# Kernel optimization log

Hardware: AMD Instinct MI355X
Metric: run time of the kernel (lower is better)

The kernel has to match this reference:

```python
import jax, jax.numpy as jnp
import numpy as np

C_S = 384; C_Z = 256; HD = 16; NH = 12; NQ = 4; NV = 8; L = 512
WC = float(np.sqrt(2.0 / (9.0 * NQ)))
WL = float(np.sqrt(1.0 / 3.0))


def quat2rot(q):
    # q: [L,4] -> R: [L,3,3] (normalized quaternion to rotation matrix)
    q = q / jnp.linalg.norm(q, axis=-1, keepdims=True)
    w, x, y, z = q[..., 0], q[..., 1], q[..., 2], q[..., 3]
    R = jnp.stack([
        1 - 2 * (y * y + z * z), 2 * (x * y - w * z), 2 * (x * z + w * y),
        2 * (x * y + w * z), 1 - 2 * (x * x + z * z), 2 * (y * z - w * x),
        2 * (x * z - w * y), 2 * (y * z + w * x), 1 - 2 * (x * x + y * y)
    ], axis=-1)
    return R.reshape(q.shape[:-1] + (3, 3))


def _layer_norm(x, g, b, eps=1e-5):
    m = x.mean(-1, keepdims=True)
    v = x.var(-1, keepdims=True)
    return (x - m) / jnp.sqrt(v + eps) * g + b


def setup_inputs() -> dict:
    key = jax.random.key(0)
    ks = jax.random.split(key, 20)
    f32 = jnp.float32
    def w(k, shape, fan_in):
        return (jax.random.normal(k, shape) / np.sqrt(fan_in)).astype(f32)
    shid = NH * (C_Z + HD + NV * 3 + NV)  # 3648
    return {
        "s": jax.random.normal(ks[0], (1, L, C_S), f32),
        "z": jax.random.normal(ks[1], (1, L, L, C_Z), f32),
        "quat_tns": jax.random.normal(ks[2], (1, L, 4), f32),
        "trsl_tns": jax.random.normal(ks[3], (1, L, 3), f32),
        "Wq": w(ks[4], (C_S, NH * HD), C_S),
        "Wk": w(ks[5], (C_S, NH * HD), C_S),
        "Wv": w(ks[6], (C_S, NH * HD), C_S),
        "Wqp": w(ks[7], (C_S, NH * NQ * 3), C_S),
        "Wkp": w(ks[8], (C_S, NH * NQ * 3), C_S),
        "Wvp": w(ks[9], (C_S, NH * NV * 3), C_S),
        "Wb": w(ks[10], (C_Z, NH), C_Z),
        "Ws": w(ks[11], (shid, C_S), shid),
        "bs": jnp.zeros((C_S,), f32),
        "scale": jnp.full((NH,), np.log(np.e - 1.0), f32),
        "g1": jnp.ones((C_S,), f32), "b1": jnp.zeros((C_S,), f32),
        "Wm1": w(ks[12], (C_S, C_S), C_S), "bm1": jnp.zeros((C_S,), f32),
        "Wm2": w(ks[13], (C_S, C_S), C_S), "bm2": jnp.zeros((C_S,), f32),
        "Wm3": w(ks[14], (C_S, C_S), C_S), "bm3": jnp.zeros((C_S,), f32),
        "g2": jnp.ones((C_S,), f32), "b2": jnp.zeros((C_S,), f32),
    }


def reference(s, z, quat_tns, trsl_tns, Wq, Wk, Wv, Wqp, Wkp, Wvp, Wb, Ws, bs,
              scale, g1, b1, Wm1, bm1, Wm2, bm2, Wm3, bm3, g2, b2):
    N, Lr, _ = s.shape
    q = (s @ Wq).reshape(N, Lr, NH, HD)
    k = (s @ Wk).reshape(N, Lr, NH, HD)
    v = (s @ Wv).reshape(N, Lr, NH, HD)
    qp = (s @ Wqp).reshape(N, Lr, NH, NQ, 3)
    kp = (s @ Wkp).reshape(N, Lr, NH, NQ, 3)
    vp = (s @ Wvp).reshape(N, Lr, NH, NV, 3)
    b = z @ Wb                                   # [N,L,L,H]
    R = quat2rot(quat_tns[0])[None]              # [1,L,3,3]
    t = trsl_tns[:, :, None, None, :]            # [1,L,1,1,3]

    def fwd_trans(x):                            # global frame: R x + t
        return jnp.einsum('nlij,nlhpj->nlhpi', R, x) + t

    qpp = fwd_trans(qp)                          # [N,L,H,Q,3]
    kpp = fwd_trans(kp)
    vpp = fwd_trans(vp)                          # [N,L,H,V,3]

    # sum over points and coords of squared distances -> [N,L,L,H]
    d2 = jnp.sum((qpp[:, :, None] - kpp[:, None, :]) ** 2, axis=(-1, -2))
    qk = jnp.einsum('nihd,njhd->nijh', q, k) / np.sqrt(HD)
    qkp = 0.5 * WC * jax.nn.softplus(scale)[None, None, None, :] * d2
    a = jax.nn.softmax(WL * (qk + b - qkp), axis=2)  # softmax over keys j

    op = jnp.einsum('nijh,nijc->nihc', a, z)         # [N,L,H,C_Z]
    ov = jnp.einsum('nijh,njhd->nihd', a, v)         # [N,L,H,HD]
    ovp_g = jnp.einsum('nijh,njhp->nihp', a, vpp.reshape(N, Lr, NH, NV * 3))
    ovp_g = ovp_g.reshape(N, Lr, NH, NV, 3)
    # inverse transform: R^T (y - t)
    ovp = jnp.einsum('nlji,nlhvj->nlhvi', R, ovp_g - t)
    ovp_norm = jnp.linalg.norm(ovp, axis=-1)         # [N,L,H,V]

    shid = jnp.concatenate(
        [op, ov, ovp.reshape(N, Lr, NH, NV * 3), ovp_norm], axis=3
    ).reshape(N, Lr, -1)
    s1 = _layer_norm(s + shid @ Ws + bs, g1, b1)
    h = jax.nn.relu(s1 @ Wm1 + bm1)
    h = jax.nn.relu(h @ Wm2 + bm2)
    h = h @ Wm3 + bm3
    return _layer_norm(s1 + h, g2, b2)
```

## Files before the change

kernel.cpp:

```cpp
#include <hip/hip_runtime.h>
#include <math.h>

#define LSEQ 512
#define CS 384
#define CZ 256
#define HD 16
#define NH 12
#define NQ 4
#define NV 8
#define NALL 1152
#define SHID 3648
#define OFF_Q 0
#define OFF_K 192
#define OFF_V 384
#define OFF_QP 576
#define OFF_KP 720
#define OFF_VP 864

#define WC_CONST 0.2357022603955158f
#define WL_CONST 0.5773502691896258f

typedef __attribute__((ext_vector_type(8))) short bf16x8;
typedef __attribute__((ext_vector_type(4))) float f32x4;

__device__ __forceinline__ short f2bf(float f) {
  unsigned u = __builtin_bit_cast(unsigned, f);
  unsigned r = (u + 0x7FFF + ((u >> 16) & 1)) >> 16;
  return (short)r;
}

__global__ void k_prep(const float* quat, const float* trsl, const float* scale,
                       const float* Wb, float* R, float* T, float* CH,
                       unsigned short* WBP) {
  int t = threadIdx.x;
  if (t < LSEQ) {
    float w = quat[t*4+0], x = quat[t*4+1], y = quat[t*4+2], z = quat[t*4+3];
    float inv = 1.0f / sqrtf(w*w + x*x + y*y + z*z);
    w *= inv; x *= inv; y *= inv; z *= inv;
    float* r = R + t*9;
    r[0] = 1.f - 2.f*(y*y + z*z); r[1] = 2.f*(x*y - w*z);       r[2] = 2.f*(x*z + w*y);
    r[3] = 2.f*(x*y + w*z);       r[4] = 1.f - 2.f*(x*x + z*z); r[5] = 2.f*(y*z - w*x);
    r[6] = 2.f*(x*z - w*y);       r[7] = 2.f*(y*z + w*x);       r[8] = 1.f - 2.f*(x*x + y*y);
    T[t*3+0] = trsl[t*3+0]; T[t*3+1] = trsl[t*3+1]; T[t*3+2] = trsl[t*3+2];
  }
  if (t < NH) {
    float sc = scale[t];
    float sp = (sc > 20.f) ? sc : logf(1.f + expf(sc));
    CH[t] = 0.5f * WC_CONST * sp;
  }
  if (t < CZ) {
    #pragma unroll
    for (int h = 0; h < 16; h++)
      WBP[t*16 + h] = (h < NH) ? (unsigned short)f2bf(Wb[t*NH + h]) : (unsigned short)0;
  }
}

__global__ void k_concat(const float* Wq, const float* Wk, const float* Wv,
                         const float* Wqp, const float* Wkp, const float* Wvp,
                         float* Wcat) {
  int idx = blockIdx.x * 256 + threadIdx.x;
  if (idx >= CS * NALL) return;
  int r = idx / NALL, c = idx % NALL;
  float v;
  if (c < 192)       v = Wq [r*192 + c];
  else if (c < 384)  v = Wk [r*192 + (c-192)];
  else if (c < 576)  v = Wv [r*192 + (c-384)];
  else if (c < 720)  v = Wqp[r*144 + (c-576)];
  else if (c < 864)  v = Wkp[r*144 + (c-720)];
  else               v = Wvp[r*288 + (c-864)];
  Wcat[idx] = v;
}

__global__ __launch_bounds__(256) void k_gemm(
    const float* A, const float* B, float* C, const float* bias,
    int K, int lda, int ldb, int ldc, int splitk, int relu, int reluA) {
  int ks = blockIdx.z;
  int Ksub = K / splitk;
  int kbeg = ks * Ksub, kend = kbeg + Ksub;

  __shared__ __align__(16) float As[16][68];
  __shared__ __align__(16) float Bs[16][68];
  int t = threadIdx.x;
  int m0 = blockIdx.y * 64, n0 = blockIdx.x * 64;
  int arow = t >> 2,  akq = (t & 3) * 4;
  int bkk  = t >> 4,  bnq = (t & 15) * 4;
  int ty = (t >> 4) * 4, tx = (t & 15) * 4;
  float acc[4][4];
  #pragma unroll
  for (int r = 0; r < 4; r++)
    #pragma unroll
    for (int c = 0; c < 4; c++) acc[r][c] = 0.f;

  const float* aptr  = A + (long)(m0 + arow) * lda + akq;
  const float* bbase = B + n0 + bnq;
  float4 av = *(const float4*)&aptr[kbeg];
  float4 bv = *(const float4*)&bbase[(long)(kbeg + bkk) * ldb];

  for (int kb = kbeg; kb < kend; kb += 16) {
    float4 a_cur = av, b_cur = bv;
    if (reluA) {
      a_cur.x = fmaxf(a_cur.x, 0.f); a_cur.y = fmaxf(a_cur.y, 0.f);
      a_cur.z = fmaxf(a_cur.z, 0.f); a_cur.w = fmaxf(a_cur.w, 0.f);
    }
    __syncthreads();
    As[akq+0][arow] = a_cur.x; As[akq+1][arow] = a_cur.y;
    As[akq+2][arow] = a_cur.z; As[akq+3][arow] = a_cur.w;
    *(float4*)&Bs[bkk][bnq] = b_cur;
    __syncthreads();
    if (kb + 16 < kend) {
      av = *(const float4*)&aptr[kb + 16];
      bv = *(const float4*)&bbase[(long)(kb + 16 + bkk) * ldb];
    }
    #pragma unroll
    for (int kk = 0; kk < 16; kk++) {
      float4 a4 = *(float4*)&As[kk][ty];
      float4 b4 = *(float4*)&Bs[kk][tx];
      acc[0][0] += a4.x*b4.x; acc[0][1] += a4.x*b4.y; acc[0][2] += a4.x*b4.z; acc[0][3] += a4.x*b4.w;
      acc[1][0] += a4.y*b4.x; acc[1][1] += a4.y*b4.y; acc[1][2] += a4.y*b4.z; acc[1][3] += a4.y*b4.w;
      acc[2][0] += a4.z*b4.x; acc[2][1] += a4.z*b4.y; acc[2][2] += a4.z*b4.z; acc[2][3] += a4.z*b4.w;
      acc[3][0] += a4.w*b4.x; acc[3][1] += a4.w*b4.y; acc[3][2] += a4.w*b4.z; acc[3][3] += a4.w*b4.w;
    }
  }

  if (splitk == 1) {
    #pragma unroll
    for (int r = 0; r < 4; r++) {
      int m = m0 + ty + r;
      #pragma unroll
      for (int c = 0; c < 4; c++) {
        int n = n0 + tx + c;
        float v = acc[r][c] + (bias ? bias[n] : 0.f);
        if (relu) v = fmaxf(v, 0.f);
        C[(long)m * ldc + n] = v;
      }
    }
  } else {
    #pragma unroll
    for (int r = 0; r < 4; r++) {
      int m = m0 + ty + r;
      #pragma unroll
      for (int c = 0; c < 4; c++) {
        int n = n0 + tx + c;
        float v = acc[r][c] + ((ks == 0 && bias) ? bias[n] : 0.f);
        atomicAdd(&C[(long)m * ldc + n], v);
      }
    }
  }
}

__global__ void k_trans(const float* P, const float* R, const float* T,
                        float* QPP, float* KT, float* KPT, float* VBT) {
  int task = blockIdx.y;
  int idx = blockIdx.x * 256 + threadIdx.x;
  if (idx >= LSEQ * NH) return;
  int h = idx / LSEQ, l = idx % LSEQ;
  const float* r = R + l*9;
  float t0 = T[l*3], t1 = T[l*3+1], t2 = T[l*3+2];
  const float* prow = P + (long)l * NALL;
  if (task == 0) {
    #pragma unroll
    for (int pq = 0; pq < NQ; pq++) {
      const float* x = prow + OFF_QP + h*12 + pq*3;
      float a = x[0], b = x[1], c = x[2];
      float* o = QPP + l*144 + h*12 + pq*3;
      o[0] = r[0]*a + r[1]*b + r[2]*c + t0;
      o[1] = r[3]*a + r[4]*b + r[5]*c + t1;
      o[2] = r[6]*a + r[7]*b + r[8]*c + t2;
    }
    #pragma unroll
    for (int d = 0; d < HD; d++)
      KT[(h*HD + d)*LSEQ + l] = prow[OFF_K + h*HD + d];
  } else if (task == 1) {
    #pragma unroll
    for (int pq = 0; pq < NQ; pq++) {
      const float* x = prow + OFF_KP + h*12 + pq*3;
      float a = x[0], b = x[1], c = x[2];
      KPT[(h*12 + pq*3 + 0)*LSEQ + l] = r[0]*a + r[1]*b + r[2]*c + t0;
      KPT[(h*12 + pq*3 + 1)*LSEQ + l] = r[3]*a + r[4]*b + r[5]*c + t1;
      KPT[(h*12 + pq*3 + 2)*LSEQ + l] = r[6]*a + r[7]*b + r[8]*c + t2;
    }
  } else {
    #pragma unroll
    for (int d = 0; d < 16; d++)
      VBT[((long)(h*40 + d))*LSEQ + l] = prow[OFF_V + h*16 + d];
    #pragma unroll
    for (int pv = 0; pv < NV; pv++) {
      const float* x = prow + OFF_VP + h*24 + pv*3;
      float a = x[0], b = x[1], c = x[2];
      VBT[((long)(h*40 + 16 + 3*pv + 0))*LSEQ + l] = r[0]*a + r[1]*b + r[2]*c + t0;
      VBT[((long)(h*40 + 16 + 3*pv + 1))*LSEQ + l] = r[3]*a + r[4]*b + r[5]*c + t1;
      VBT[((long)(h*40 + 16 + 3*pv + 2))*LSEQ + l] = r[6]*a + r[7]*b + r[8]*c + t2;
    }
  }
}

#define AI 2
__global__ __launch_bounds__(512) void k_logit(const float* P, const float* QPP,
    const float* KT, const float* KPT, const float* CH, float* LG) {
  int i0 = blockIdx.x * AI;
  int t = threadIdx.x, j = t;
  #pragma unroll
  for (int h = 0; h < NH; h++) {
    float kreg[16];
    #pragma unroll
    for (int d = 0; d < 16; d++) kreg[d] = KT[(h*16 + d)*LSEQ + j];
    float kp[12];
    #pragma unroll
    for (int p = 0; p < 12; p++) kp[p] = KPT[(h*12 + p)*LSEQ + j];
    float ch = CH[h];
    #pragma unroll
    for (int ii = 0; ii < AI; ii++) {
      const float* q  = P + (long)(i0+ii)*NALL + OFF_Q + h*HD;
      const float* qp = QPP + (i0+ii)*144 + h*12;
      float dot = 0.f;
      #pragma unroll
      for (int d = 0; d < 16; d++) dot += q[d] * kreg[d];
      float d2 = 0.f;
      #pragma unroll
      for (int p = 0; p < 12; p++) { float dd = qp[p] - kp[p]; d2 += dd*dd; }
      LG[((long)(i0+ii)*NH + h)*LSEQ + j] = WL_CONST * (0.25f*dot - ch*d2);
    }
  }
}

__global__ __launch_bounds__(256) void k_fused(const float* zin,
    const unsigned short* WBP, const float* LG, const float* VBT,
    float* SH, float* OVT) {
  __shared__ __align__(16) float lgs[NH][520];
  __shared__ __align__(16) float es[NH][68];
  __shared__ float sred[4][NH];
  __shared__ float ssum[NH];
  int i = blockIdx.x, t = threadIdx.x;
  int w = t >> 6, l = t & 63;
  int r = l & 15, kg = l >> 4;

  const float* lgsrc = LG + (long)i * NH * LSEQ;
  #pragma unroll
  for (int idx = t; idx < NH*LSEQ/4; idx += 256) {
    int h = idx >> 7, q4 = idx & 127;
    *(float4*)&lgs[h][q4*4] = *(const float4*)&lgsrc[h*LSEQ + q4*4];
  }

  bf16x8 bfrag[8];
  #pragma unroll
  for (int kt = 0; kt < 8; kt++)
    #pragma unroll
    for (int jj = 0; jj < 8; jj++)
      bfrag[kt][jj] = (short)WBP[(kt*32 + kg*8 + jj)*16 + r];

  float accop[NH];
  #pragma unroll
  for (int h = 0; h < NH; h++) accop[h] = 0.f;
  int pair0 = t, pair1 = t + 256;
  int h0 = pair0 / 40, p0 = pair0 % 40;
  int h1 = pair1 / 40, p1 = pair1 % 40;
  float accv0 = 0.f, accv1 = 0.f;
  float sparts = 0.f;
  int hh = (r < NH) ? r : 0;

  __syncthreads();

  for (int jt = 0; jt < LSEQ; jt += 64) {
    int j0 = jt + w*16;
    const float* zrow = zin + ((long)i*LSEQ + j0 + r)*CZ + kg*8;
    f32x4 acc = {0.f, 0.f, 0.f, 0.f};
    #pragma unroll
    for (int kt = 0; kt < 8; kt++) {
      float4 z0 = *(const float4*)(zrow + kt*32);
      float4 z1 = *(const float4*)(zrow + kt*32 + 4);
      bf16x8 af;
      af[0] = f2bf(z0.x); af[1] = f2bf(z0.y); af[2] = f2bf(z0.z); af[3] = f2bf(z0.w);
      af[4] = f2bf(z1.x); af[5] = f2bf(z1.y); af[6] = f2bf(z1.z); af[7] = f2bf(z1.w);
      acc = __builtin_amdgcn_mfma_f32_16x16x32_bf16(af, bfrag[kt], acc, 0, 0, 0);
    }
    float4 lgv = *(float4*)&lgs[hh][j0 + kg*4];
    float e0 = __expf(lgv.x + WL_CONST*acc[0]);
    float e1 = __expf(lgv.y + WL_CONST*acc[1]);
    float e2 = __expf(lgv.z + WL_CONST*acc[2]);
    float e3 = __expf(lgv.w + WL_CONST*acc[3]);
    if (r < NH) {
      sparts += e0 + e1 + e2 + e3;
      *(float4*)&es[r][w*16 + kg*4] = make_float4(e0, e1, e2, e3);
    }
    __syncthreads();
    const float* zc = zin + ((long)i*LSEQ + jt)*CZ + t;
    #pragma unroll 4
    for (int jj = 0; jj < 64; jj += 4) {
      float z0 = zc[(jj+0)*CZ], z1 = zc[(jj+1)*CZ];
      float z2 = zc[(jj+2)*CZ], z3 = zc[(jj+3)*CZ];
      #pragma unroll
      for (int h = 0; h < NH; h++) {
        float4 ev = *(float4*)&es[h][jj];
        accop[h] += ev.x*z0 + ev.y*z1 + ev.z*z2 + ev.w*z3;
      }
    }
    {
      const float* vb0 = VBT + ((long)pair0)*LSEQ + jt;
      #pragma unroll
      for (int jj = 0; jj < 64; jj += 4) {
        float4 vv = *(const float4*)&vb0[jj];
        float4 ev = *(float4*)&es[h0][jj];
        accv0 += vv.x*ev.x + vv.y*ev.y + vv.z*ev.z + vv.w*ev.w;
      }
      if (pair1 < 480) {
        const float* vb1 = VBT + ((long)pair1)*LSEQ + jt;
        #pragma unroll
        for (int jj = 0; jj < 64; jj += 4) {
          float4 vv = *(const float4*)&vb1[jj];
          float4 ev = *(float4*)&es[h1][jj];
          accv1 += vv.x*ev.x + vv.y*ev.y + vv.z*ev.z + vv.w*ev.w;
        }
      }
    }
    __syncthreads();
  }

  sparts += __shfl_xor(sparts, 16);
  sparts += __shfl_xor(sparts, 32);
  if (l < NH) sred[w][l] = sparts;
  __syncthreads();
  if (t < NH) {
    float sv = sred[0][t] + sred[1][t] + sred[2][t] + sred[3][t];
    ssum[t] = 1.0f / sv;
  }
  __syncthreads();

  float* sh = SH + (long)i * SHID + t;
  #pragma unroll
  for (int h = 0; h < NH; h++) sh[h * 304] = accop[h] * ssum[h];
  OVT[(long)i*480 + pair0] = accv0 * ssum[h0];
  if (pair1 < 480) OVT[(long)i*480 + pair1] = accv1 * ssum[h1];
}

__global__ void k_ovp(const float* OVT, const float* R, const float* T, float* SH) {
  int idx = blockIdx.x * 256 + threadIdx.x;
  if (idx >= LSEQ * NH) return;
  int l = idx / NH, h = idx % NH;
  const float* o = OVT + (long)l*480 + h*40;
  float* sh = SH + (long)l * SHID + h * 304;
  #pragma unroll
  for (int d = 0; d < 16; d++) sh[256 + d] = o[d];
  const float* r = R + l*9;
  float t0 = T[l*3], t1 = T[l*3+1], t2 = T[l*3+2];
  #pragma unroll
  for (int v = 0; v < NV; v++) {
    float a = o[16+3*v+0] - t0, b = o[16+3*v+1] - t1, c = o[16+3*v+2] - t2;
    float x = r[0]*a + r[3]*b + r[6]*c;
    float y = r[1]*a + r[4]*b + r[7]*c;
    float zz= r[2]*a + r[5]*b + r[8]*c;
    sh[272 + 3*v + 0] = x;
    sh[272 + 3*v + 1] = y;
    sh[272 + 3*v + 2] = zz;
    sh[296 + v] = sqrtf(x*x + y*y + zz*zz);
  }
}

__global__ __launch_bounds__(384) void k_ln(const float* res, const float* y,
                                            const float* g, const float* b, float* out) {
  int l = blockIdx.x, t = threadIdx.x;
  __shared__ float red1[6], red2[6];
  __shared__ float mv[2];
  float x = res[(long)l * CS + t] + y[(long)l * CS + t];
  float s = x, s2 = x * x;
  #pragma unroll
  for (int off = 32; off >= 1; off >>= 1) { s += __shfl_xor(s, off); s2 += __shfl_xor(s2, off); }
  if ((t & 63) == 0) { red1[t >> 6] = s; red2[t >> 6] = s2; }
  __syncthreads();
  if (t == 0) {
    float ss = 0.f, ss2 = 0.f;
    #pragma unroll
    for (int u = 0; u < 6; u++) { ss += red1[u]; ss2 += red2[u]; }
    float m = ss / CS;
    float var = ss2 / CS - m * m;
    mv[0] = m; mv[1] = 1.0f / sqrtf(var + 1e-5f);
  }
  __syncthreads();
  out[(long)l * CS + t] = (x - mv[0]) * mv[1] * g[t] + b[t];
}

extern "C" void kernel_launch(void* const* d_in, const int* in_sizes, int n_in,
                              void* d_out, int out_size, void* d_ws, size_t ws_size,
                              hipStream_t stream) {
  const float* s    = (const float*)d_in[0];
  const float* z    = (const float*)d_in[1];
  const float* quat = (const float*)d_in[2];
  const float* trsl = (const float*)d_in[3];
  const float* Wq   = (const float*)d_in[4];
  const float* Wk   = (const float*)d_in[5];
  const float* Wv   = (const float*)d_in[6];
  const float* Wqp  = (const float*)d_in[7];
  const float* Wkp  = (const float*)d_in[8];
  const float* Wvp  = (const float*)d_in[9];
  const float* Wb   = (const float*)d_in[10];
  const float* Ws   = (const float*)d_in[11];
  const float* bs   = (const float*)d_in[12];
  const float* scale= (const float*)d_in[13];
  const float* g1   = (const float*)d_in[14];
  const float* b1   = (const float*)d_in[15];
  const float* Wm1  = (const float*)d_in[16];
  const float* bm1  = (const float*)d_in[17];
  const float* Wm2  = (const float*)d_in[18];
  const float* bm2  = (const float*)d_in[19];
  const float* Wm3  = (const float*)d_in[20];
  const float* bm3  = (const float*)d_in[21];
  const float* g2   = (const float*)d_in[22];
  const float* b2   = (const float*)d_in[23];
  float* out = (float*)d_out;

  float* p = (float*)d_ws;
  float* R    = p; p += 512*9;
  float* T    = p; p += 512*3;
  float* CH   = p; p += 16;
  unsigned short* WBP = (unsigned short*)p; p += (CZ*16)/2;
  float* Wcat = p; p += (long)CS*NALL;
  float* QPP  = p; p += LSEQ*144;
  float* KT   = p; p += NH*HD*LSEQ;
  float* KPT  = p; p += NH*12*LSEQ;
  float* VBT  = p; p += (long)NH*40*LSEQ;
  float* LG   = p; p += (long)LSEQ*NH*LSEQ;
  float* OVT  = p; p += (long)LSEQ*480;
  float* SH   = p; p += (long)LSEQ*SHID;
  float* S1   = p; p += LSEQ*CS;
  float* ZB   = p;
  float* P    = p; p += (long)LSEQ*NALL;
  float* T1   = p; p += LSEQ*CS;
  float* H1   = p; p += LSEQ*CS;
  float* H2   = p; p += LSEQ*CS;
  float* H3   = p; p += LSEQ*CS;
  size_t zbytes = ((size_t)LSEQ*NALL + 4*LSEQ*CS) * sizeof(float);

  hipMemsetAsync(ZB, 0, zbytes, stream);
  k_prep<<<1, 512, 0, stream>>>(quat, trsl, scale, Wb, R, T, CH, WBP);
  k_concat<<<(CS*NALL + 255)/256, 256, 0, stream>>>(Wq, Wk, Wv, Wqp, Wkp, Wvp, Wcat);
  k_gemm<<<dim3(NALL/64, LSEQ/64, 2), 256, 0, stream>>>(
      s, Wcat, P, nullptr, CS, CS, NALL, NALL, 2, 0, 0);
  k_trans<<<dim3(24, 3), 256, 0, stream>>>(P, R, T, QPP, KT, KPT, VBT);
  k_logit<<<LSEQ/AI, 512, 0, stream>>>(P, QPP, KT, KPT, CH, LG);
  k_fused<<<LSEQ, 256, 0, stream>>>(z, WBP, LG, VBT, SH, OVT);
  k_ovp<<<(LSEQ*NH + 255)/256, 256, 0, stream>>>(OVT, R, T, SH);
  k_gemm<<<dim3(CS/64, LSEQ/64, 12), 256, 0, stream>>>(
      SH, Ws, T1, bs, SHID, SHID, CS, CS, 12, 0, 0);
  k_ln<<<LSEQ, CS, 0, stream>>>(s, T1, g1, b1, S1);
  k_gemm<<<dim3(CS/64, LSEQ/64, 8), 256, 0, stream>>>(
      S1, Wm1, H1, bm1, CS, CS, CS, CS, 8, 0, 0);
  k_gemm<<<dim3(CS/64, LSEQ/64, 8), 256, 0, stream>>>(
      H1, Wm2, H2, bm2, CS, CS, CS, CS, 8, 0, 1);
  k_gemm<<<dim3(CS/64, LSEQ/64, 8), 256, 0, stream>>>(
      H2, Wm3, H3, bm3, CS, CS, CS, CS, 8, 0, 1);
  k_ln<<<LSEQ, CS, 0, stream>>>(S1, H3, g2, b2, out);
}
```

Measured before the change: 690.6 us.

## Split attention key dimension across two blocks with atomic accumulation

The fused attention/z-aggregation kernel now launches a 512x2 grid, each block handling half of the keys, and accumulates unnormalized outputs and softmax denominators via atomicAdd into zeroed buffers. A new normalization kernel divides op by the summed denominators, and k_ovp applies the same division to the value outputs. The logit kernel is also changed to one query row per block. This aims to raise occupancy and parallelism for the z-bound kernel, at the cost of atomics, a larger memset and an extra launch. It relies on no per-row max subtraction, which the code before also skipped.

```diff
diff --git a/kernel.cpp b/kernel.cpp
--- a/kernel.cpp
+++ b/kernel.cpp
@@ -194,11 +194,10 @@
   }
 }
 
-#define AI 2
 __global__ __launch_bounds__(512) void k_logit(const float* P, const float* QPP,
     const float* KT, const float* KPT, const float* CH, float* LG) {
-  int i0 = blockIdx.x * AI;
-  int t = threadIdx.x, j = t;
+  int i = blockIdx.x;
+  int j = threadIdx.x;
   #pragma unroll
   for (int h = 0; h < NH; h++) {
     float kreg[16];
@@ -208,36 +207,33 @@
     #pragma unroll
     for (int p = 0; p < 12; p++) kp[p] = KPT[(h*12 + p)*LSEQ + j];
     float ch = CH[h];
-    #pragma unroll
-    for (int ii = 0; ii < AI; ii++) {
-      const float* q  = P + (long)(i0+ii)*NALL + OFF_Q + h*HD;
-      const float* qp = QPP + (i0+ii)*144 + h*12;
-      float dot = 0.f;
-      #pragma unroll
-      for (int d = 0; d < 16; d++) dot += q[d] * kreg[d];
-      float d2 = 0.f;
-      #pragma unroll
-      for (int p = 0; p < 12; p++) { float dd = qp[p] - kp[p]; d2 += dd*dd; }
-      LG[((long)(i0+ii)*NH + h)*LSEQ + j] = WL_CONST * (0.25f*dot - ch*d2);
-    }
+    const float* q  = P + (long)i*NALL + OFF_Q + h*HD;
+    const float* qp = QPP + i*144 + h*12;
+    float dot = 0.f;
+    #pragma unroll
+    for (int d = 0; d < 16; d++) dot += q[d] * kreg[d];
+    float d2 = 0.f;
+    #pragma unroll
+    for (int p = 0; p < 12; p++) { float dd = qp[p] - kp[p]; d2 += dd*dd; }
+    LG[((long)i*NH + h)*LSEQ + j] = WL_CONST * (0.25f*dot - ch*d2);
   }
 }
 
 __global__ __launch_bounds__(256) void k_fused(const float* zin,
     const unsigned short* WBP, const float* LG, const float* VBT,
-    float* SH, float* OVT) {
-  __shared__ __align__(16) float lgs[NH][520];
+    float* SH, float* OVT, float* SSUM) {
+  __shared__ __align__(16) float lgs[NH][264];
   __shared__ __align__(16) float es[NH][68];
   __shared__ float sred[4][NH];
-  __shared__ float ssum[NH];
-  int i = blockIdx.x, t = threadIdx.x;
+  int i = blockIdx.x, js = blockIdx.y, t = threadIdx.x;
+  int jbase = js * 256;
   int w = t >> 6, l = t & 63;
   int r = l & 15, kg = l >> 4;
 
-  const float* lgsrc = LG + (long)i * NH * LSEQ;
-  #pragma unroll
-  for (int idx = t; idx < NH*LSEQ/4; idx += 256) {
-    int h = idx >> 7, q4 = idx & 127;
+  const float* lgsrc = LG + (long)i * NH * LSEQ + jbase;
+  #pragma unroll
+  for (int idx = t; idx < NH*256/4; idx += 256) {
+    int h = idx >> 6, q4 = idx & 63;
     *(float4*)&lgs[h][q4*4] = *(const float4*)&lgsrc[h*LSEQ + q4*4];
   }
 
@@ -252,17 +248,18 @@
   #pragma unroll
   for (int h = 0; h < NH; h++) accop[h] = 0.f;
   int pair0 = t, pair1 = t + 256;
-  int h0 = pair0 / 40, p0 = pair0 % 40;
-  int h1 = pair1 / 40, p1 = pair1 % 40;
+  int h0 = pair0 / 40;
+  int h1 = pair1 / 40;
   float accv0 = 0.f, accv1 = 0.f;
   float sparts = 0.f;
   int hh = (r < NH) ? r : 0;
 
   __syncthreads();
 
-  for (int jt = 0; jt < LSEQ; jt += 64) {
+  for (int jt = 0; jt < 256; jt += 64) {
     int j0 = jt + w*16;
-    const float* zrow = zin + ((long)i*LSEQ + j0 + r)*CZ + kg*8;
+    int j0g = jbase + j0;
+    const float* zrow = zin + ((long)i*LSEQ + j0g + r)*CZ + kg*8;
     f32x4 acc = {0.f, 0.f, 0.f, 0.f};
     #pragma unroll
     for (int kt = 0; kt < 8; kt++) {
@@ -283,7 +280,7 @@
       *(float4*)&es[r][w*16 + kg*4] = make_float4(e0, e1, e2, e3);
     }
     __syncthreads();
-    const float* zc = zin + ((long)i*LSEQ + jt)*CZ + t;
+    const float* zc = zin + ((long)i*LSEQ + jbase + jt)*CZ + t;
     #pragma unroll 4
     for (int jj = 0; jj < 64; jj += 4) {
       float z0 = zc[(jj+0)*CZ], z1 = zc[(jj+1)*CZ];
@@ -295,7 +292,7 @@
       }
     }
     {
-      const float* vb0 = VBT + ((long)pair0)*LSEQ + jt;
+      const float* vb0 = VBT + ((long)pair0)*LSEQ + jbase + jt;
       #pragma unroll
       for (int jj = 0; jj < 64; jj += 4) {
         float4 vv = *(const float4*)&vb0[jj];
@@ -303,7 +300,7 @@
         accv0 += vv.x*ev.x + vv.y*ev.y + vv.z*ev.z + vv.w*ev.w;
       }
       if (pair1 < 480) {
-        const float* vb1 = VBT + ((long)pair1)*LSEQ + jt;
+        const float* vb1 = VBT + ((long)pair1)*LSEQ + jbase + jt;
         #pragma unroll
         for (int jj = 0; jj < 64; jj += 4) {
           float4 vv = *(const float4*)&vb1[jj];
@@ -319,32 +316,41 @@
   sparts += __shfl_xor(sparts, 32);
   if (l < NH) sred[w][l] = sparts;
   __syncthreads();
-  if (t < NH) {
-    float sv = sred[0][t] + sred[1][t] + sred[2][t] + sred[3][t];
-    ssum[t] = 1.0f / sv;
-  }
-  __syncthreads();
+  if (t < NH)
+    atomicAdd(&SSUM[i*16 + t], sred[0][t] + sred[1][t] + sred[2][t] + sred[3][t]);
 
   float* sh = SH + (long)i * SHID + t;
   #pragma unroll
-  for (int h = 0; h < NH; h++) sh[h * 304] = accop[h] * ssum[h];
-  OVT[(long)i*480 + pair0] = accv0 * ssum[h0];
-  if (pair1 < 480) OVT[(long)i*480 + pair1] = accv1 * ssum[h1];
-}
-
-__global__ void k_ovp(const float* OVT, const float* R, const float* T, float* SH) {
+  for (int h = 0; h < NH; h++) atomicAdd(&sh[h * 304], accop[h]);
+  atomicAdd(&OVT[(long)i*480 + pair0], accv0);
+  if (pair1 < 480) atomicAdd(&OVT[(long)i*480 + pair1], accv1);
+}
+
+__global__ __launch_bounds__(256) void k_opnorm(const float* SSUM, float* SH) {
+  int i = blockIdx.x, t = threadIdx.x;
+  float* sh = SH + (long)i * SHID + t;
+  #pragma unroll
+  for (int h = 0; h < NH; h++) {
+    float inv = 1.0f / SSUM[i*16 + h];
+    sh[h * 304] *= inv;
+  }
+}
+
+__global__ void k_ovp(const float* OVT, const float* SSUM, const float* R,
+                      const float* T, float* SH) {
   int idx = blockIdx.x * 256 + threadIdx.x;
   if (idx >= LSEQ * NH) return;
   int l = idx / NH, h = idx % NH;
+  float inv = 1.0f / SSUM[l*16 + h];
   const float* o = OVT + (long)l*480 + h*40;
   float* sh = SH + (long)l * SHID + h * 304;
   #pragma unroll
-  for (int d = 0; d < 16; d++) sh[256 + d] = o[d];
+  for (int d = 0; d < 16; d++) sh[256 + d] = o[d] * inv;
   const float* r = R + l*9;
   float t0 = T[l*3], t1 = T[l*3+1], t2 = T[l*3+2];
   #pragma unroll
   for (int v = 0; v < NV; v++) {
-    float a = o[16+3*v+0] - t0, b = o[16+3*v+1] - t1, c = o[16+3*v+2] - t2;
+    float a = o[16+3*v+0]*inv - t0, b = o[16+3*v+1]*inv - t1, c = o[16+3*v+2]*inv - t2;
     float x = r[0]*a + r[3]*b + r[6]*c;
     float y = r[1]*a + r[4]*b + r[7]*c;
     float zz= r[2]*a + r[5]*b + r[8]*c;
@@ -418,8 +424,6 @@
   float* KPT  = p; p += NH*12*LSEQ;
   float* VBT  = p; p += (long)NH*40*LSEQ;
   float* LG   = p; p += (long)LSEQ*NH*LSEQ;
-  float* OVT  = p; p += (long)LSEQ*480;
-  float* SH   = p; p += (long)LSEQ*SHID;
   float* S1   = p; p += LSEQ*CS;
   float* ZB   = p;
   float* P    = p; p += (long)LSEQ*NALL;
@@ -427,7 +431,11 @@
   float* H1   = p; p += LSEQ*CS;
   float* H2   = p; p += LSEQ*CS;
   float* H3   = p; p += LSEQ*CS;
-  size_t zbytes = ((size_t)LSEQ*NALL + 4*LSEQ*CS) * sizeof(float);
+  float* SH   = p; p += (long)LSEQ*SHID;
+  float* OVT  = p; p += (long)LSEQ*480;
+  float* SSUM = p; p += LSEQ*16;
+  size_t zbytes = ((size_t)LSEQ*NALL + 4*LSEQ*CS + (size_t)LSEQ*SHID
+                   + (size_t)LSEQ*480 + LSEQ*16) * sizeof(float);
 
   hipMemsetAsync(ZB, 0, zbytes, stream);
   k_prep<<<1, 512, 0, stream>>>(quat, trsl, scale, Wb, R, T, CH, WBP);
@@ -435,9 +443,10 @@
   k_gemm<<<dim3(NALL/64, LSEQ/64, 2), 256, 0, stream>>>(
       s, Wcat, P, nullptr, CS, CS, NALL, NALL, 2, 0, 0);
   k_trans<<<dim3(24, 3), 256, 0, stream>>>(P, R, T, QPP, KT, KPT, VBT);
-  k_logit<<<LSEQ/AI, 512, 0, stream>>>(P, QPP, KT, KPT, CH, LG);
-  k_fused<<<LSEQ, 256, 0, stream>>>(z, WBP, LG, VBT, SH, OVT);
-  k_ovp<<<(LSEQ*NH + 255)/256, 256, 0, stream>>>(OVT, R, T, SH);
+  k_logit<<<LSEQ, 512, 0, stream>>>(P, QPP, KT, KPT, CH, LG);
+  k_fused<<<dim3(LSEQ, 2), 256, 0, stream>>>(z, WBP, LG, VBT, SH, OVT, SSUM);
+  k_opnorm<<<LSEQ, 256, 0, stream>>>(SSUM, SH);
+  k_ovp<<<(LSEQ*NH + 255)/256, 256, 0, stream>>>(OVT, SSUM, R, T, SH);
   k_gemm<<<dim3(CS/64, LSEQ/64, 12), 256, 0, stream>>>(
       SH, Ws, T1, bs, SHID, SHID, CS, CS, 12, 0, 0);
   k_ln<<<LSEQ, CS, 0, stream>>>(s, T1, g1, b1, S1);
```

Result: no change. 698.8 us (+1.2%).

## Fuse logit, attention and point-output kernels into one 512-thread kernel

Applied to the files above, without the earlier changes.

Folds the logit computation and the inverse-frame point transform into the main attention kernel, so the LG and OVT global intermediates and two launches are removed. Each block now has 512 threads split into two groups, each handling half of the key positions. The partial sums are combined through shared memory at the end. The per-step second barrier is replaced by double-buffered exp tiles. This removes the 12 MB logit round-trip, but each block now recomputes its own logits and needs more shared memory per block, which may lower occupancy.

```diff
diff --git a/kernel.cpp b/kernel.cpp
--- a/kernel.cpp
+++ b/kernel.cpp
@@ -194,51 +194,49 @@
   }
 }
 
-#define AI 2
-__global__ __launch_bounds__(512) void k_logit(const float* P, const float* QPP,
-    const float* KT, const float* KPT, const float* CH, float* LG) {
-  int i0 = blockIdx.x * AI;
-  int t = threadIdx.x, j = t;
-  #pragma unroll
-  for (int h = 0; h < NH; h++) {
-    float kreg[16];
-    #pragma unroll
-    for (int d = 0; d < 16; d++) kreg[d] = KT[(h*16 + d)*LSEQ + j];
-    float kp[12];
-    #pragma unroll
-    for (int p = 0; p < 12; p++) kp[p] = KPT[(h*12 + p)*LSEQ + j];
-    float ch = CH[h];
-    #pragma unroll
-    for (int ii = 0; ii < AI; ii++) {
-      const float* q  = P + (long)(i0+ii)*NALL + OFF_Q + h*HD;
-      const float* qp = QPP + (i0+ii)*144 + h*12;
+__global__ __launch_bounds__(512) void k_fused512(
+    const float* zin, const unsigned short* WBP, const float* P,
+    const float* QPP, const float* KT, const float* KPT, const float* CH,
+    const float* VBT, const float* R, const float* T, float* SH) {
+  __shared__ __align__(16) float smem[12864];
+  float (*lgs)[516] = (float (*)[516])smem;
+  float (*es)[2][NH][68] = (float (*)[2][NH][68])(smem + 6192);
+  float* sred   = smem + 6192 + 6528;
+  float* ssumv  = sred + 128;
+  float* red_op = smem + 6192;
+  float* red_v  = smem + 6192 + 3072;
+
+  int i = blockIdx.x, t = threadIdx.x;
+  int g = t >> 8;
+  int w8 = t >> 6;
+  int wg = w8 & 3;
+  int l = t & 63, r = l & 15, kg = l >> 4;
+  int cidx = t & 255;
+  int hh = (r < NH) ? r : 0;
+
+  {
+    int j = t;
+    const float* qb  = P + (long)i*NALL + OFF_Q;
+    const float* qpb = QPP + i*144;
+    #pragma unroll 2
+    for (int h = 0; h < NH; h++) {
+      float kreg[16];
+      #pragma unroll
+      for (int d = 0; d < 16; d++) kreg[d] = KT[(h*16 + d)*LSEQ + j];
+      float kp[12];
+      #pragma unroll
+      for (int p = 0; p < 12; p++) kp[p] = KPT[(h*12 + p)*LSEQ + j];
+      float ch = CH[h];
+      const float* q  = qb + h*HD;
+      const float* qp = qpb + h*12;
       float dot = 0.f;
       #pragma unroll
       for (int d = 0; d < 16; d++) dot += q[d] * kreg[d];
       float d2 = 0.f;
       #pragma unroll
       for (int p = 0; p < 12; p++) { float dd = qp[p] - kp[p]; d2 += dd*dd; }
-      LG[((long)(i0+ii)*NH + h)*LSEQ + j] = WL_CONST * (0.25f*dot - ch*d2);
-    }
-  }
-}
-
-__global__ __launch_bounds__(256) void k_fused(const float* zin,
-    const unsigned short* WBP, const float* LG, const float* VBT,
-    float* SH, float* OVT) {
-  __shared__ __align__(16) float lgs[NH][520];
-  __shared__ __align__(16) float es[NH][68];
-  __shared__ float sred[4][NH];
-  __shared__ float ssum[NH];
-  int i = blockIdx.x, t = threadIdx.x;
-  int w = t >> 6, l = t & 63;
-  int r = l & 15, kg = l >> 4;
-
-  const float* lgsrc = LG + (long)i * NH * LSEQ;
-  #pragma unroll
-  for (int idx = t; idx < NH*LSEQ/4; idx += 256) {
-    int h = idx >> 7, q4 = idx & 127;
-    *(float4*)&lgs[h][q4*4] = *(const float4*)&lgsrc[h*LSEQ + q4*4];
+      lgs[h][j] = WL_CONST * (0.25f*dot - ch*d2);
+    }
   }
 
   bf16x8 bfrag[8];
@@ -251,17 +249,17 @@
   float accop[NH];
   #pragma unroll
   for (int h = 0; h < NH; h++) accop[h] = 0.f;
-  int pair0 = t, pair1 = t + 256;
-  int h0 = pair0 / 40, p0 = pair0 % 40;
-  int h1 = pair1 / 40, p1 = pair1 % 40;
+  int pair0 = cidx, pair1 = cidx + 256;
+  int h0 = pair0 / 40, h1 = pair1 / 40;
   float accv0 = 0.f, accv1 = 0.f;
   float sparts = 0.f;
-  int hh = (r < NH) ? r : 0;
-
-  __syncthreads();
-
-  for (int jt = 0; jt < LSEQ; jt += 64) {
-    int j0 = jt + w*16;
+
+  __syncthreads();
+
+  int buf = 0;
+  for (int step = 0; step < 4; step++) {
+    int jt = step * 64;
+    int j0 = g*256 + jt + wg*16;
     const float* zrow = zin + ((long)i*LSEQ + j0 + r)*CZ + kg*8;
     f32x4 acc = {0.f, 0.f, 0.f, 0.f};
     #pragma unroll
@@ -280,78 +278,93 @@
     float e3 = __expf(lgv.w + WL_CONST*acc[3]);
     if (r < NH) {
       sparts += e0 + e1 + e2 + e3;
-      *(float4*)&es[r][w*16 + kg*4] = make_float4(e0, e1, e2, e3);
+      *(float4*)&es[g][buf][r][wg*16 + kg*4] = make_float4(e0, e1, e2, e3);
     }
     __syncthreads();
-    const float* zc = zin + ((long)i*LSEQ + jt)*CZ + t;
+    const float* zc = zin + ((long)i*LSEQ + g*256 + jt)*CZ + cidx;
     #pragma unroll 4
     for (int jj = 0; jj < 64; jj += 4) {
       float z0 = zc[(jj+0)*CZ], z1 = zc[(jj+1)*CZ];
       float z2 = zc[(jj+2)*CZ], z3 = zc[(jj+3)*CZ];
       #pragma unroll
       for (int h = 0; h < NH; h++) {
-        float4 ev = *(float4*)&es[h][jj];
+        float4 ev = *(float4*)&es[g][buf][h][jj];
         accop[h] += ev.x*z0 + ev.y*z1 + ev.z*z2 + ev.w*z3;
       }
     }
     {
-      const float* vb0 = VBT + ((long)pair0)*LSEQ + jt;
+      const float* vb0 = VBT + ((long)pair0)*LSEQ + g*256 + jt;
       #pragma unroll
       for (int jj = 0; jj < 64; jj += 4) {
         float4 vv = *(const float4*)&vb0[jj];
-        float4 ev = *(float4*)&es[h0][jj];
+        float4 ev = *(float4*)&es[g][buf][h0][jj];
         accv0 += vv.x*ev.x + vv.y*ev.y + vv.z*ev.z + vv.w*ev.w;
       }
       if (pair1 < 480) {
-        const float* vb1 = VBT + ((long)pair1)*LSEQ + jt;
+        const float* vb1 = VBT + ((long)pair1)*LSEQ + g*256 + jt;
         #pragma unroll
         for (int jj = 0; jj < 64; jj += 4) {
           float4 vv = *(const float4*)&vb1[jj];
-          float4 ev = *(float4*)&es[h1][jj];
+          float4 ev = *(float4*)&es[g][buf][h1][jj];
           accv1 += vv.x*ev.x + vv.y*ev.y + vv.z*ev.z + vv.w*ev.w;
         }
       }
     }
-    __syncthreads();
+    buf ^= 1;
   }
 
   sparts += __shfl_xor(sparts, 16);
   sparts += __shfl_xor(sparts, 32);
-  if (l < NH) sred[w][l] = sparts;
-  __syncthreads();
+  if (l < NH) sred[w8*16 + l] = sparts;
+  __syncthreads();
+
+  if (g == 1) {
+    #pragma unroll
+    for (int h = 0; h < NH; h++) red_op[h*256 + cidx] = accop[h];
+    red_v[pair0] = accv0;
+    if (pair1 < 480) red_v[pair1] = accv1;
+  }
   if (t < NH) {
-    float sv = sred[0][t] + sred[1][t] + sred[2][t] + sred[3][t];
-    ssum[t] = 1.0f / sv;
-  }
-  __syncthreads();
-
-  float* sh = SH + (long)i * SHID + t;
-  #pragma unroll
-  for (int h = 0; h < NH; h++) sh[h * 304] = accop[h] * ssum[h];
-  OVT[(long)i*480 + pair0] = accv0 * ssum[h0];
-  if (pair1 < 480) OVT[(long)i*480 + pair1] = accv1 * ssum[h1];
-}
-
-__global__ void k_ovp(const float* OVT, const float* R, const float* T, float* SH) {
-  int idx = blockIdx.x * 256 + threadIdx.x;
-  if (idx >= LSEQ * NH) return;
-  int l = idx / NH, h = idx % NH;
-  const float* o = OVT + (long)l*480 + h*40;
-  float* sh = SH + (long)l * SHID + h * 304;
-  #pragma unroll
-  for (int d = 0; d < 16; d++) sh[256 + d] = o[d];
-  const float* r = R + l*9;
-  float t0 = T[l*3], t1 = T[l*3+1], t2 = T[l*3+2];
-  #pragma unroll
-  for (int v = 0; v < NV; v++) {
-    float a = o[16+3*v+0] - t0, b = o[16+3*v+1] - t1, c = o[16+3*v+2] - t2;
-    float x = r[0]*a + r[3]*b + r[6]*c;
-    float y = r[1]*a + r[4]*b + r[7]*c;
-    float zz= r[2]*a + r[5]*b + r[8]*c;
-    sh[272 + 3*v + 0] = x;
-    sh[272 + 3*v + 1] = y;
-    sh[272 + 3*v + 2] = zz;
-    sh[296 + v] = sqrtf(x*x + y*y + zz*zz);
+    float sv = 0.f;
+    #pragma unroll
+    for (int u = 0; u < 8; u++) sv += sred[u*16 + t];
+    ssumv[t] = 1.0f / sv;
+  }
+  __syncthreads();
+
+  if (g == 0) {
+    float* sh = SH + (long)i * SHID + cidx;
+    #pragma unroll
+    for (int h = 0; h < NH; h++)
+      sh[h * 304] = (accop[h] + red_op[h*256 + cidx]) * ssumv[h];
+    float v0 = (accv0 + red_v[pair0]) * ssumv[h0];
+    red_v[pair0] = v0;
+    if (pair1 < 480) {
+      float v1 = (accv1 + red_v[pair1]) * ssumv[h1];
+      red_v[pair1] = v1;
+    }
+  }
+  __syncthreads();
+
+  if (t < NH) {
+    int h = t;
+    const float* rr = R + i*9;
+    float t0 = T[i*3], t1 = T[i*3+1], t2 = T[i*3+2];
+    float* sh = SH + (long)i * SHID + h*304;
+    const float* o = red_v + h*40;
+    #pragma unroll
+    for (int d = 0; d < 16; d++) sh[256 + d] = o[d];
+    #pragma unroll
+    for (int v = 0; v < NV; v++) {
+      float a = o[16+3*v+0] - t0, b = o[16+3*v+1] - t1, c = o[16+3*v+2] - t2;
+      float x = rr[0]*a + rr[3]*b + rr[6]*c;
+      float y = rr[1]*a + rr[4]*b + rr[7]*c;
+      float zz= rr[2]*a + rr[5]*b + rr[8]*c;
+      sh[272 + 3*v + 0] = x;
+      sh[272 + 3*v + 1] = y;
+      sh[272 + 3*v + 2] = zz;
+      sh[296 + v] = sqrtf(x*x + y*y + zz*zz);
+    }
   }
 }
 
@@ -417,8 +430,6 @@
   float* KT   = p; p += NH*HD*LSEQ;
   float* KPT  = p; p += NH*12*LSEQ;
   float* VBT  = p; p += (long)NH*40*LSEQ;
-  float* LG   = p; p += (long)LSEQ*NH*LSEQ;
-  float* OVT  = p; p += (long)LSEQ*480;
   float* SH   = p; p += (long)LSEQ*SHID;
   float* S1   = p; p += LSEQ*CS;
   float* ZB   = p;
@@ -435,9 +446,7 @@
   k_gemm<<<dim3(NALL/64, LSEQ/64, 2), 256, 0, stream>>>(
       s, Wcat, P, nullptr, CS, CS, NALL, NALL, 2, 0, 0);
   k_trans<<<dim3(24, 3), 256, 0, stream>>>(P, R, T, QPP, KT, KPT, VBT);
-  k_logit<<<LSEQ/AI, 512, 0, stream>>>(P, QPP, KT, KPT, CH, LG);
-  k_fused<<<LSEQ, 256, 0, stream>>>(z, WBP, LG, VBT, SH, OVT);
-  k_ovp<<<(LSEQ*NH + 255)/256, 256, 0, stream>>>(OVT, R, T, SH);
+  k_fused512<<<LSEQ, 512, 0, stream>>>(z, WBP, P, QPP, KT, KPT, CH, VBT, R, T, SH);
   k_gemm<<<dim3(CS/64, LSEQ/64, 12), 256, 0, stream>>>(
       SH, Ws, T1, bs, SHID, SHID, CS, CS, 12, 0, 0);
   k_ln<<<LSEQ, CS, 0, stream>>>(s, T1, g1, b1, S1);
```

Result: no change. 691.8 us (+0.2%).
